# Kernel optimization log

Measured on AMD Instinct MI355X. Metric: run time of the kernel, lower is better.

Reference implementation:

```python
import jax, jax.numpy as jnp
import numpy as np

U, D, E, L = 100000, 10000, 500000, 100000
H, O, VC = 128, 64, 20
ED = H // 4  # emb_dim = hidden // 4


def setup_inputs() -> dict:
    key = jax.random.key(0)
    it = iter(jax.random.split(key, 60))
    def nrm(shape, s=0.1):
        return jax.random.normal(next(it), shape, jnp.float32) * s
    inp = {}
    inp["x_user"] = nrm((U, 3), 1.0)
    inp["x_dest"] = nrm((D, 1), 1.0)
    inp["edge_src"] = jax.random.randint(next(it), (E,), 0, U)
    inp["edge_dst"] = jax.random.randint(next(it), (E,), 0, D)
    inp["eattr_cat"] = jax.random.randint(next(it), (E, 3), 0, VC)
    inp["eattr_num"] = nrm((E, 3), 1.0)
    inp["label_src"] = jax.random.randint(next(it), (L,), 0, U)
    inp["label_dst"] = jax.random.randint(next(it), (L,), 0, D)
    inp["user_emb"] = nrm((U, H))
    inp["dest_emb"] = nrm((D, H))
    inp["Wuf"] = nrm((3, H)); inp["buf"] = jnp.zeros((H,), jnp.float32)
    inp["Wdf"] = nrm((1, H)); inp["bdf"] = jnp.zeros((H,), jnp.float32)
    inp["emb_acc"] = nrm((VC, ED)); inp["emb_trans"] = nrm((VC, ED)); inp["emb_season"] = nrm((VC, ED))
    inp["Wnum"] = nrm((3, ED)); inp["bnum"] = jnp.zeros((ED,), jnp.float32)
    inp["Weout"] = nrm((4 * ED, H)); inp["beout"] = jnp.zeros((H,), jnp.float32)
    inp["c1v_Ws"] = nrm((H, H)); inp["c1v_Wd"] = nrm((H, H)); inp["c1v_as"] = nrm((H,)); inp["c1v_ad"] = nrm((H,))
    inp["c1v_We"] = nrm((H, H)); inp["c1v_ae"] = nrm((H,)); inp["c1v_b"] = jnp.zeros((H,), jnp.float32)
    inp["c1r_Ws"] = nrm((H, H)); inp["c1r_Wd"] = nrm((H, H)); inp["c1r_as"] = nrm((H,)); inp["c1r_ad"] = nrm((H,)); inp["c1r_b"] = jnp.zeros((H,), jnp.float32)
    inp["c2v_W"] = nrm((H, H)); inp["c2v_as"] = nrm((H,)); inp["c2v_ad"] = nrm((H,)); inp["c2v_We"] = nrm((H, H)); inp["c2v_ae"] = nrm((H,)); inp["c2v_b"] = jnp.zeros((H,), jnp.float32)
    inp["c2r_W"] = nrm((H, H)); inp["c2r_as"] = nrm((H,)); inp["c2r_ad"] = nrm((H,)); inp["c2r_b"] = jnp.zeros((H,), jnp.float32)
    inp["Wmu"] = nrm((H, O)); inp["bmu"] = jnp.zeros((O,), jnp.float32)
    inp["Wls"] = nrm((H, O)); inp["bls"] = jnp.zeros((O,), jnp.float32)
    return inp


def gat(h_src, h_dst, src, dst, Ws, Wd, a_s, a_d, bias, n_dst, ef=None, We=None, ae=None):
    """PyG GATConv, heads=1, add_self_loops=False, bipartite (src->dst)."""
    xs = h_src @ Ws  # [Ns, H]
    xd = h_dst @ Wd  # [Nd, H]
    alpha = (xs * a_s).sum(-1)[src] + (xd * a_d).sum(-1)[dst]  # [E]
    if ef is not None:
        alpha = alpha + ((ef @ We) * ae).sum(-1)
    alpha = jnp.where(alpha > 0, alpha, 0.2 * alpha)  # leaky_relu(0.2)
    amax = jax.ops.segment_max(alpha, dst, num_segments=n_dst)
    ex = jnp.exp(alpha - amax[dst])
    denom = jax.ops.segment_sum(ex, dst, num_segments=n_dst)
    w = ex / (denom[dst] + 1e-16)  # segment softmax over incoming edges
    out = jax.ops.segment_sum(w[:, None] * xs[src], dst, num_segments=n_dst)
    return out + bias


def reference(x_user, x_dest, edge_src, edge_dst, eattr_cat, eattr_num, label_src, label_dst,
              user_emb, dest_emb, Wuf, buf, Wdf, bdf,
              emb_acc, emb_trans, emb_season, Wnum, bnum, Weout, beout,
              c1v_Ws, c1v_Wd, c1v_as, c1v_ad, c1v_We, c1v_ae, c1v_b,
              c1r_Ws, c1r_Wd, c1r_as, c1r_ad, c1r_b,
              c2v_W, c2v_as, c2v_ad, c2v_We, c2v_ae, c2v_b,
              c2r_W, c2r_as, c2r_ad, c2r_b,
              Wmu, bmu, Wls, bls):
    # node encoders (full-batch: arange ids == full embedding tables)
    h_user = user_emb + x_user @ Wuf + buf  # [U, H]
    h_dest = dest_emb + x_dest @ Wdf + bdf  # [D, H]
    # EdgeBehaviorEncoder
    ef = jnp.concatenate([emb_acc[eattr_cat[:, 0]], emb_trans[eattr_cat[:, 1]],
                          emb_season[eattr_cat[:, 2]], eattr_num @ Wnum + bnum], axis=1)
    ef = ef @ Weout + beout  # [E, H]
    # layer 1
    od1 = gat(h_user, h_dest, edge_src, edge_dst, c1v_Ws, c1v_Wd, c1v_as, c1v_ad, c1v_b, D, ef, c1v_We, c1v_ae)
    ou1 = gat(h_dest, h_user, edge_dst, edge_src, c1r_Ws, c1r_Wd, c1r_as, c1r_ad, c1r_b, U)
    hu = jax.nn.relu(ou1)
    hd = jax.nn.relu(od1)
    # layer 2 (int in_channels -> shared lin for src and dst)
    od2 = gat(hu, hd, edge_src, edge_dst, c2v_W, c2v_W, c2v_as, c2v_ad, c2v_b, D, ef, c2v_We, c2v_ae)
    ou2 = gat(hd, hu, edge_dst, edge_src, c2r_W, c2r_W, c2r_as, c2r_ad, c2r_b, U)
    zu = jax.nn.relu(ou2)
    zd = jax.nn.relu(od2)
    mu_u = zu @ Wmu + bmu
    mu_d = zd @ Wmu + bmu
    ls_u = zu @ Wls + bls
    ls_d = zd @ Wls + bls
    # eval mode: reparameterize returns mu; decode = dot product on label edges
    pred = (mu_u[label_src] * mu_d[label_dst]).sum(-1)  # [L]
    return pred, mu_u, mu_d, ls_u, ls_d
```

## Files before the change

kernel.cpp:

```cpp
#include <hip/hip_runtime.h>
#include <hip/hip_bf16.h>
#include <math.h>

#define H 128
#define CDIV(a,b) (((a)+(b)-1)/(b))

__device__ __forceinline__ float wave_reduce_sum(float v){
  #pragma unroll
  for (int off = 32; off > 0; off >>= 1) v += __shfl_down(v, off, 64);
  return v;
}
__device__ __forceinline__ float wave_reduce_max(float v){
  #pragma unroll
  for (int off = 32; off > 0; off >>= 1) v = fmaxf(v, __shfl_xor(v, off, 64));
  return v;
}

__global__ __launch_bounds__(128) void k_precompute(
    const float* c1v_Wd, const float* c1v_ad,
    const float* c1r_Wd, const float* c1r_ad,
    const float* c2v_W,  const float* c2v_ad,
    const float* c2r_W,  const float* c2r_ad,
    const float* c1v_We, const float* c1v_ae,
    const float* c2v_We, const float* c2v_ae,
    const float* Weout,  const float* beout,
    const float* emb_acc, const float* emb_trans, const float* emb_season,
    const float* Wnum, const float* bnum,
    const float* Wmu, const float* Wls, const float* bmu, const float* bls,
    float* sm)
{
  const int b = blockIdx.x, t = threadIdx.x;
  if (b < 4){
    const float* M; const float* a;
    if      (b == 0){ M = c1v_Wd; a = c1v_ad; }
    else if (b == 1){ M = c1r_Wd; a = c1r_ad; }
    else if (b == 2){ M = c2v_W;  a = c2v_ad; }
    else            { M = c2r_W;  a = c2r_ad; }
    float s = 0.f;
    for (int j = 0; j < H; ++j) s += M[t*H+j] * a[j];
    sm[b*H + t] = s;
  } else if (b == 4){
    __shared__ float ws[H], vs[H];
    for (int layer = 0; layer < 2; ++layer){
      const float* We = layer ? c2v_We : c1v_We;
      const float* ae = layer ? c2v_ae : c1v_ae;
      float w = 0.f;
      for (int j = 0; j < H; ++j) w += We[t*H+j] * ae[j];
      ws[t] = w;
      __syncthreads();
      float v = 0.f;
      for (int j = 0; j < H; ++j) v += Weout[t*H+j] * ws[j];
      vs[t] = v;
      __syncthreads();
      float* tab = sm + 512 + layer*64;
      if (t < 20){
        float s1 = 0.f, s2 = 0.f, s3 = 0.f;
        for (int i = 0; i < 32; ++i){
          s1 += emb_acc   [t*32+i] * vs[i];
          s2 += emb_trans [t*32+i] * vs[32+i];
          s3 += emb_season[t*32+i] * vs[64+i];
        }
        tab[t] = s1; tab[20+t] = s2; tab[40+t] = s3;
      }
      if (t < 3){
        float s = 0.f;
        for (int i = 0; i < 32; ++i) s += Wnum[t*32+i] * vs[96+i];
        tab[60+t] = s;
      }
      if (t == 0){
        float s = 0.f;
        for (int j = 0; j < H; ++j)  s += beout[j] * ws[j];
        for (int i = 0; i < 32; ++i) s += bnum[i] * vs[96+i];
        tab[63] = s;
      }
      __syncthreads();
    }
  } else {
    float* Wcat = sm + 768;
    for (int i = (b-5)*128 + t; i < 8192; i += 7*128){
      int h = i >> 6, o = i & 63;
      Wcat[h*H + o]      = Wmu[h*64 + o];
      Wcat[h*H + 64 + o] = Wls[h*64 + o];
    }
    if (b == 5) sm[640 + t] = (t < 64) ? bmu[t] : bls[t-64];
  }
}

__global__ __launch_bounds__(256) void k_enc_user(
    const float* __restrict__ emb, const float* __restrict__ x,
    const float* __restrict__ Wf, const float* __restrict__ b,
    const float* __restrict__ qd, float* __restrict__ out,
    float* __restrict__ sout, int N)
{
  int w = (blockIdx.x*blockDim.x + threadIdx.x) >> 6;
  int lane = threadIdx.x & 63;
  if (w >= N) return;
  const float2* emb2 = (const float2*)emb;
  const float2* Wf2  = (const float2*)Wf;
  float2 e  = emb2[(size_t)w*64 + lane];
  float x0 = x[w*3], x1 = x[w*3+1], x2 = x[w*3+2];
  float2 w0 = Wf2[lane], w1 = Wf2[64+lane], w2 = Wf2[128+lane];
  float2 bb = ((const float2*)b)[lane];
  float h0 = e.x + bb.x + x0*w0.x + x1*w1.x + x2*w2.x;
  float h1 = e.y + bb.y + x0*w0.y + x1*w1.y + x2*w2.y;
  ((float2*)out)[(size_t)w*64 + lane] = make_float2(h0, h1);
  float2 q = ((const float2*)qd)[lane];
  float p = wave_reduce_sum(h0*q.x + h1*q.y);
  if (lane == 0) sout[w] = p;
}

__global__ __launch_bounds__(256) void k_enc_dest(
    const float* __restrict__ emb, const float* __restrict__ x,
    const float* __restrict__ Wf, const float* __restrict__ b,
    const float* __restrict__ qd, float* __restrict__ out,
    float* __restrict__ sout, int N)
{
  int w = (blockIdx.x*blockDim.x + threadIdx.x) >> 6;
  int lane = threadIdx.x & 63;
  if (w >= N) return;
  float2 e  = ((const float2*)emb)[(size_t)w*64 + lane];
  float x0 = x[w];
  float2 w0 = ((const float2*)Wf)[lane];
  float2 bb = ((const float2*)b)[lane];
  float h0 = e.x + bb.x + x0*w0.x;
  float h1 = e.y + bb.y + x0*w0.y;
  ((float2*)out)[(size_t)w*64 + lane] = make_float2(h0, h1);
  float2 q = ((const float2*)qd)[lane];
  float p = wave_reduce_sum(h0*q.x + h1*q.y);
  if (lane == 0) sout[w] = p;
}

__global__ __launch_bounds__(256) void k_gemm128(
    const float* __restrict__ A, const float* __restrict__ W,
    const float* __restrict__ bias, const float* __restrict__ asv,
    float* __restrict__ sout,
    float* __restrict__ out0, float* __restrict__ out1,
    int ld0, int ld1, int N)
{
  __shared__ float Ws[64][128];
  __shared__ float Xs[64][132];
  __shared__ float red[64][17];
  const int tid = threadIdx.x;
  const int rb  = blockIdx.x * 64;
  const int tc  = tid & 15, tr = tid >> 4;
  const int c0  = tc * 8;
  float C[4][8] = {};
  for (int k0 = 0; k0 < 128; k0 += 64){
    for (int i = tid; i < 2048; i += 256){
      int k = i >> 5, c4 = i & 31;
      *(float4*)&Ws[k][c4*4] = *(const float4*)&W[(size_t)(k0+k)*128 + c4*4];
    }
    for (int i = tid; i < 1024; i += 256){
      int r = i >> 4, kg = i & 15;
      int row = rb + r;
      float4 v = make_float4(0.f,0.f,0.f,0.f);
      if (row < N) v = *(const float4*)&A[(size_t)row*128 + k0 + kg*4];
      *(float4*)&Xs[r][kg*4] = v;
    }
    __syncthreads();
    #pragma unroll 4
    for (int k = 0; k < 64; ++k){
      float4 w0 = *(float4*)&Ws[k][c0];
      float4 w1 = *(float4*)&Ws[k][c0+4];
      #pragma unroll
      for (int i = 0; i < 4; ++i){
        float x = Xs[tr*4+i][k];
        C[i][0] += x*w0.x; C[i][1] += x*w0.y; C[i][2] += x*w0.z; C[i][3] += x*w0.w;
        C[i][4] += x*w1.x; C[i][5] += x*w1.y; C[i][6] += x*w1.z; C[i][7] += x*w1.w;
      }
    }
    __syncthreads();
  }
  float4 b0 = make_float4(0,0,0,0), b1 = make_float4(0,0,0,0);
  if (bias){ b0 = *(const float4*)&bias[c0]; b1 = *(const float4*)&bias[c0+4]; }
  float4 a0 = make_float4(0,0,0,0), a1 = make_float4(0,0,0,0);
  if (asv){ a0 = *(const float4*)&asv[c0]; a1 = *(const float4*)&asv[c0+4]; }
  #pragma unroll
  for (int i = 0; i < 4; ++i){
    int row = rb + tr*4 + i;
    float s = 0.f;
    if (row < N){
      float4 v0 = make_float4(C[i][0]+b0.x, C[i][1]+b0.y, C[i][2]+b0.z, C[i][3]+b0.w);
      float4 v1 = make_float4(C[i][4]+b1.x, C[i][5]+b1.y, C[i][6]+b1.z, C[i][7]+b1.w);
      if (c0 < 64){
        *(float4*)&out0[(size_t)row*ld0 + c0]     = v0;
        *(float4*)&out0[(size_t)row*ld0 + c0 + 4] = v1;
      } else {
        *(float4*)&out1[(size_t)row*ld1 + (c0-64)]     = v0;
        *(float4*)&out1[(size_t)row*ld1 + (c0-64) + 4] = v1;
      }
      if (asv){
        s = C[i][0]*a0.x + C[i][1]*a0.y + C[i][2]*a0.z + C[i][3]*a0.w
          + C[i][4]*a1.x + C[i][5]*a1.y + C[i][6]*a1.z + C[i][7]*a1.w;
      }
    }
    if (asv) red[tr*4+i][tc] = s;
  }
  if (asv){
    __syncthreads();
    if (tid < 64){
      int row = rb + tid;
      if (row < N){
        float t = 0.f;
        #pragma unroll
        for (int j = 0; j < 16; ++j) t += red[tid][j];
        sout[row] = t;
      }
    }
  }
}

__global__ __launch_bounds__(256) void k_alpha_both(
    const int* __restrict__ esrc, const int* __restrict__ edst,
    const int* __restrict__ ecat, const float* __restrict__ enum_,
    const float* __restrict__ sUa, const float* __restrict__ sDa,
    const float* __restrict__ sDb, const float* __restrict__ sUb,
    const float* __restrict__ tab,
    const int* __restrict__ slotD, const int* __restrict__ slotU,
    float* __restrict__ alVs, float* __restrict__ alRs, int E)
{
  int e = blockIdx.x * blockDim.x + threadIdx.x;
  if (e >= E) return;
  int s = esrc[e], d = edst[e];
  float av = sUa[s] + sDa[d]
           + tab[ecat[e*3]] + tab[20 + ecat[e*3+1]] + tab[40 + ecat[e*3+2]]
           + enum_[e*3]*tab[60] + enum_[e*3+1]*tab[61] + enum_[e*3+2]*tab[62] + tab[63];
  av = av > 0.f ? av : 0.2f * av;
  alVs[slotD[e]] = av;
  float ar = sDb[d] + sUb[s];
  ar = ar > 0.f ? ar : 0.2f * ar;
  alRs[slotU[e]] = ar;
}

__global__ void k_zero2(int* a, int na, int* b, int nb){
  int i = blockIdx.x * blockDim.x + threadIdx.x;
  if (i < na) a[i] = 0;
  else if (i - na < nb) b[i - na] = 0;
}

__global__ void k_count_both(const int* __restrict__ esrc, const int* __restrict__ edst,
                             int* __restrict__ cntU, int* __restrict__ cntD, int E){
  int e = blockIdx.x * blockDim.x + threadIdx.x;
  if (e < E){ atomicAdd(&cntU[esrc[e]], 1); atomicAdd(&cntD[edst[e]], 1); }
}

__global__ __launch_bounds__(1024) void k_scan1(const int* __restrict__ cnt,
                                                int* __restrict__ offs,
                                                int* __restrict__ bsum, int n)
{
  __shared__ int wsum[16];
  const int tid = threadIdx.x, lane = tid & 63, wid = tid >> 6;
  const int i = blockIdx.x * 1024 + tid;
  int v = (i < n) ? cnt[i] : 0;
  int inc = v;
  #pragma unroll
  for (int d = 1; d < 64; d <<= 1){
    int t2 = __shfl_up(inc, d, 64);
    if (lane >= d) inc += t2;
  }
  if (lane == 63) wsum[wid] = inc;
  __syncthreads();
  if (tid < 16){
    int x = wsum[tid];
    #pragma unroll
    for (int d = 1; d < 16; d <<= 1){
      int t2 = __shfl_up(x, d, 16);
      if (tid >= d) x += t2;
    }
    wsum[tid] = x;
  }
  __syncthreads();
  int incl = ((wid > 0) ? wsum[wid-1] : 0) + inc;
  if (i < n) offs[i+1] = incl;
  if (tid == 0) bsum[blockIdx.x] = wsum[15];
}

__global__ __launch_bounds__(1024) void k_scan2(int* __restrict__ bsum, int nb)
{
  __shared__ int wsum[16];
  const int tid = threadIdx.x, lane = tid & 63, wid = tid >> 6;
  int v = (tid < nb) ? bsum[tid] : 0;
  int inc = v;
  #pragma unroll
  for (int d = 1; d < 64; d <<= 1){
    int t2 = __shfl_up(inc, d, 64);
    if (lane >= d) inc += t2;
  }
  if (lane == 63) wsum[wid] = inc;
  __syncthreads();
  if (tid < 16){
    int x = wsum[tid];
    #pragma unroll
    for (int d = 1; d < 16; d <<= 1){
      int t2 = __shfl_up(x, d, 16);
      if (tid >= d) x += t2;
    }
    wsum[tid] = x;
  }
  __syncthreads();
  int excl = ((wid > 0) ? wsum[wid-1] : 0) + inc - v;
  if (tid < nb) bsum[tid] = excl;
}

__global__ void k_scan3(const int* __restrict__ cnt, const int* __restrict__ bsum,
                        int* __restrict__ offs, int* __restrict__ cursor, int n)
{
  int i = blockIdx.x * blockDim.x + threadIdx.x;
  if (i >= n) return;
  int v = offs[i+1] + bsum[i >> 10];
  offs[i+1] = v;
  cursor[i] = v - cnt[i];
  if (i == 0) offs[0] = 0;
}

__global__ void k_scatter_both(const int* __restrict__ esrc, const int* __restrict__ edst,
                               int* __restrict__ curU, int* __restrict__ curD,
                               int* __restrict__ slotU, int* __restrict__ slotD,
                               int* __restrict__ srtOU, int* __restrict__ srtOD, int E)
{
  int e = blockIdx.x * blockDim.x + threadIdx.x;
  if (e >= E) return;
  int s = esrc[e], d = edst[e];
  int pD = atomicAdd(&curD[d], 1);
  slotD[e] = pD; srtOD[pD] = s;
  int pU = atomicAdd(&curU[s], 1);
  slotU[e] = pU; srtOU[pU] = d;
}

__global__ __launch_bounds__(256) void k_agg(
    const int* __restrict__ offs, const int* __restrict__ srt_other,
    const float* __restrict__ al, const float* __restrict__ xs,
    const float* __restrict__ bias, float* __restrict__ out,
    const float* __restrict__ qd, float* __restrict__ sout, int N)
{
  int w = (blockIdx.x*blockDim.x + threadIdx.x) >> 6;
  int lane = threadIdx.x & 63;
  if (w >= N) return;
  const int beg = offs[w], end = offs[w+1];

  float m = -1e30f;
  for (int i = beg + lane; i < end; i += 64) m = fmaxf(m, al[i]);
  m = wave_reduce_max(m);
  float s = 0.f;
  for (int i = beg + lane; i < end; i += 64) s += __expf(al[i] - m);
  s = wave_reduce_sum(s);
  s = __shfl(s, 0, 64);
  const float inv = 1.f / (s + 1e-16f);

  float a0 = 0.f, a1 = 0.f;
  const float2* xs2 = (const float2*)xs;
  for (int base = beg; base < end; base += 64){
    int nn = min(64, end - base);
    int o_l = 0; float w_l = 0.f;
    if (base + lane < end){
      o_l = srt_other[base + lane];
      w_l = __expf(al[base + lane] - m) * inv;
    }
    for (int j = 0; j < nn; ++j){
      int   oo = __shfl(o_l, j, 64);
      float ww = __shfl(w_l, j, 64);
      float2 v = xs2[(size_t)oo*64 + lane];
      a0 += ww * v.x; a1 += ww * v.y;
    }
  }
  float2 bb = ((const float2*)bias)[lane];
  float r0 = fmaxf(a0 + bb.x, 0.f);
  float r1 = fmaxf(a1 + bb.y, 0.f);
  ((float2*)out)[(size_t)w*64 + lane] = make_float2(r0, r1);
  if (qd){
    float2 q = ((const float2*)qd)[lane];
    float p = wave_reduce_sum(r0*q.x + r1*q.y);
    if (lane == 0) sout[w] = p;
  }
}

__global__ void k_pred(const int* __restrict__ ls, const int* __restrict__ ld,
                       const float* __restrict__ mu_u, const float* __restrict__ mu_d,
                       float* __restrict__ pred, int L)
{
  int wid  = (blockIdx.x * blockDim.x + threadIdx.x) >> 6;
  int lane = threadIdx.x & 63;
  if (wid >= L) return;
  float p = mu_u[(size_t)ls[wid]*64 + lane] * mu_d[(size_t)ld[wid]*64 + lane];
  p = wave_reduce_sum(p);
  if (lane == 0) pred[wid] = p;
}

extern "C" void kernel_launch(void* const* d_in, const int* in_sizes, int n_in,
                              void* d_out, int out_size, void* d_ws, size_t ws_size,
                              hipStream_t stream)
{
  (void)n_in; (void)out_size; (void)ws_size;
  const float* x_user    = (const float*)d_in[0];
  const float* x_dest    = (const float*)d_in[1];
  const int*   edge_src  = (const int*)d_in[2];
  const int*   edge_dst  = (const int*)d_in[3];
  const int*   eattr_cat = (const int*)d_in[4];
  const float* eattr_num = (const float*)d_in[5];
  const int*   label_src = (const int*)d_in[6];
  const int*   label_dst = (const int*)d_in[7];
  const float* user_emb  = (const float*)d_in[8];
  const float* dest_emb  = (const float*)d_in[9];
  const float* Wuf = (const float*)d_in[10]; const float* buf_ = (const float*)d_in[11];
  const float* Wdf = (const float*)d_in[12]; const float* bdf  = (const float*)d_in[13];
  const float* emb_acc    = (const float*)d_in[14];
  const float* emb_trans  = (const float*)d_in[15];
  const float* emb_season = (const float*)d_in[16];
  const float* Wnum = (const float*)d_in[17]; const float* bnum  = (const float*)d_in[18];
  const float* Weout = (const float*)d_in[19]; const float* beout = (const float*)d_in[20];
  const float* c1v_Ws = (const float*)d_in[21]; const float* c1v_Wd = (const float*)d_in[22];
  const float* c1v_as = (const float*)d_in[23]; const float* c1v_ad = (const float*)d_in[24];
  const float* c1v_We = (const float*)d_in[25]; const float* c1v_ae = (const float*)d_in[26];
  const float* c1v_b  = (const float*)d_in[27];
  const float* c1r_Ws = (const float*)d_in[28]; const float* c1r_Wd = (const float*)d_in[29];
  const float* c1r_as = (const float*)d_in[30]; const float* c1r_ad = (const float*)d_in[31];
  const float* c1r_b  = (const float*)d_in[32];
  const float* c2v_W  = (const float*)d_in[33]; const float* c2v_as = (const float*)d_in[34];
  const float* c2v_ad = (const float*)d_in[35]; const float* c2v_We = (const float*)d_in[36];
  const float* c2v_ae = (const float*)d_in[37]; const float* c2v_b  = (const float*)d_in[38];
  const float* c2r_W  = (const float*)d_in[39]; const float* c2r_as = (const float*)d_in[40];
  const float* c2r_ad = (const float*)d_in[41]; const float* c2r_b  = (const float*)d_in[42];
  const float* Wmu = (const float*)d_in[43]; const float* bmu = (const float*)d_in[44];
  const float* Wls = (const float*)d_in[45]; const float* bls = (const float*)d_in[46];

  const int U = in_sizes[0] / 3;
  const int D = in_sizes[1];
  const int E = in_sizes[2];
  const int L = in_sizes[6];
  const int O = 64;
  const int nbD = CDIV(D, 1024), nbU = CDIV(U, 1024);

  float* fw = (float*)d_ws;
  size_t off = 0;
  auto falloc = [&](size_t n)->float*{ float* p = fw + off; off += (n + 3) & ~(size_t)3; return p; };
  float* A    = falloc((size_t)U * H);
  float* BIG  = falloc((size_t)U * H);
  float* Bd   = falloc((size_t)D * H);
  float* SM   = falloc((size_t)D * H);
  float* alVs = falloc(E);
  float* alRs = falloc(E);
  float* sUa  = falloc(U);
  float* sUb  = falloc(U);
  float* sDa  = falloc(D);
  float* sDb  = falloc(D);
  float* sml  = falloc(17152);
  int* iw = (int*)(fw + off);
  size_t ioff = 0;
  auto ialloc = [&](size_t n)->int*{ int* p = iw + ioff; ioff += (n + 3) & ~(size_t)3; return p; };
  int* cntD  = ialloc(D);
  int* curD  = ialloc(D);
  int* offsD = ialloc((size_t)D + 1);
  int* cntU  = ialloc(U);
  int* curU  = ialloc(U);
  int* offsU = ialloc((size_t)U + 1);
  int* slotD = ialloc(E);
  int* slotU = ialloc(E);
  int* srtOD = ialloc(E);
  int* srtOU = ialloc(E);
  int* bsumD = ialloc(1024);
  int* bsumU = ialloc(1024);

  float* outp = (float*)d_out;
  float* pred = outp;
  float* mu_u = outp + L;
  float* mu_d = mu_u + (size_t)U * O;
  float* ls_u = mu_d + (size_t)D * O;
  float* ls_d = ls_u + (size_t)U * O;

  hipLaunchKernelGGL(k_precompute, dim3(12), dim3(128), 0, stream,
                     c1v_Wd, c1v_ad, c1r_Wd, c1r_ad, c2v_W, c2v_ad, c2r_W, c2r_ad,
                     c1v_We, c1v_ae, c2v_We, c2v_ae, Weout, beout,
                     emb_acc, emb_trans, emb_season, Wnum, bnum, Wmu, Wls, bmu, bls, sml);
  hipLaunchKernelGGL(k_enc_user, dim3(CDIV(U,4)), dim3(256), 0, stream,
                     user_emb, x_user, Wuf, buf_, sml+128, A, sUb, U);
  hipLaunchKernelGGL(k_enc_dest, dim3(CDIV(D,4)), dim3(256), 0, stream,
                     dest_emb, x_dest, Wdf, bdf, sml+0, Bd, sDa, D);

  hipLaunchKernelGGL(k_zero2, dim3(CDIV(U+D,256)), dim3(256), 0, stream, cntU, U, cntD, D);
  hipLaunchKernelGGL(k_count_both, dim3(CDIV(E,256)), dim3(256), 0, stream,
                     edge_src, edge_dst, cntU, cntD, E);
  hipLaunchKernelGGL(k_scan1, dim3(nbD), dim3(1024), 0, stream, cntD, offsD, bsumD, D);
  hipLaunchKernelGGL(k_scan1, dim3(nbU), dim3(1024), 0, stream, cntU, offsU, bsumU, U);
  hipLaunchKernelGGL(k_scan2, dim3(1), dim3(1024), 0, stream, bsumD, nbD);
  hipLaunchKernelGGL(k_scan2, dim3(1), dim3(1024), 0, stream, bsumU, nbU);
  hipLaunchKernelGGL(k_scan3, dim3(CDIV(D,256)), dim3(256), 0, stream, cntD, bsumD, offsD, curD, D);
  hipLaunchKernelGGL(k_scan3, dim3(CDIV(U,256)), dim3(256), 0, stream, cntU, bsumU, offsU, curU, U);
  hipLaunchKernelGGL(k_scatter_both, dim3(CDIV(E,256)), dim3(256), 0, stream,
                     edge_src, edge_dst, curU, curD, slotU, slotD, srtOU, srtOD, E);

  hipLaunchKernelGGL(k_gemm128, dim3(CDIV(U,64)), dim3(256), 0, stream,
                     A,  c1v_Ws, (const float*)nullptr, c1v_as, sUa, BIG, BIG+64, 128, 128, U);
  hipLaunchKernelGGL(k_gemm128, dim3(CDIV(D,64)), dim3(256), 0, stream,
                     Bd, c1r_Ws, (const float*)nullptr, c1r_as, sDb, SM, SM+64, 128, 128, D);
  hipLaunchKernelGGL(k_alpha_both, dim3(CDIV(E,256)), dim3(256), 0, stream,
                     edge_src, edge_dst, eattr_cat, eattr_num, sUa, sDa, sDb, sUb,
                     sml+512, slotD, slotU, alVs, alRs, E);
  hipLaunchKernelGGL(k_agg, dim3(CDIV(D,4)), dim3(256), 0, stream,
                     offsD, srtOD, alVs, BIG, c1v_b, Bd, sml+256, sDa, D);
  hipLaunchKernelGGL(k_agg, dim3(CDIV(U,4)), dim3(256), 0, stream,
                     offsU, srtOU, alRs, SM, c1r_b, A, sml+384, sUb, U);

  hipLaunchKernelGGL(k_gemm128, dim3(CDIV(U,64)), dim3(256), 0, stream,
                     A,  c2v_W, (const float*)nullptr, c2v_as, sUa, BIG, BIG+64, 128, 128, U);
  hipLaunchKernelGGL(k_gemm128, dim3(CDIV(D,64)), dim3(256), 0, stream,
                     Bd, c2r_W, (const float*)nullptr, c2r_as, sDb, SM, SM+64, 128, 128, D);
  hipLaunchKernelGGL(k_alpha_both, dim3(CDIV(E,256)), dim3(256), 0, stream,
                     edge_src, edge_dst, eattr_cat, eattr_num, sUa, sDa, sDb, sUb,
                     sml+576, slotD, slotU, alVs, alRs, E);
  hipLaunchKernelGGL(k_agg, dim3(CDIV(D,4)), dim3(256), 0, stream,
                     offsD, srtOD, alVs, BIG, c2v_b, Bd, (const float*)nullptr, (float*)nullptr, D);
  hipLaunchKernelGGL(k_agg, dim3(CDIV(U,4)), dim3(256), 0, stream,
                     offsU, srtOU, alRs, SM, c2r_b, A, (const float*)nullptr, (float*)nullptr, U);

  hipLaunchKernelGGL(k_gemm128, dim3(CDIV(U,64)), dim3(256), 0, stream,
                     A,  sml+768, sml+640, (const float*)nullptr, (float*)nullptr, mu_u, ls_u, 64, 64, U);
  hipLaunchKernelGGL(k_gemm128, dim3(CDIV(D,64)), dim3(256), 0, stream,
                     Bd, sml+768, sml+640, (const float*)nullptr, (float*)nullptr, mu_d, ls_d, 64, 64, D);
  hipLaunchKernelGGL(k_pred, dim3(CDIV((size_t)L*64,256)), dim3(256), 0, stream,
                     label_src, label_dst, mu_u, mu_d, pred, L);
}
```

Before: 916.8 us.

## Fuse attention logit computation into aggregation with precomputed edge records

Removes the separate per-edge alpha kernels that wrote logits into scattered CSR slots. The scatter kernel now stores, per destination-sorted edge, an int4 record holding the source index and the two layers' edge-attribute logit constants. The aggregation kernels recompute leaky-relu logits from the node scores using an online max/sum softmax with a wave merge. This drops the slot arrays, the logit buffers and two passes over all edges, but each logit is gathered and computed twice inside aggregation, and every D-side edge record is now 16 bytes.

```diff
diff --git a/kernel.cpp b/kernel.cpp
--- a/kernel.cpp
+++ b/kernel.cpp
@@ -10,10 +10,16 @@
   for (int off = 32; off > 0; off >>= 1) v += __shfl_down(v, off, 64);
   return v;
 }
-__device__ __forceinline__ float wave_reduce_max(float v){
+
+__device__ __forceinline__ void wave_merge_ms(float& m, float& s){
   #pragma unroll
-  for (int off = 32; off > 0; off >>= 1) v = fmaxf(v, __shfl_xor(v, off, 64));
-  return v;
+  for (int off = 32; off > 0; off >>= 1){
+    float m2 = __shfl_xor(m, off, 64);
+    float s2 = __shfl_xor(s, off, 64);
+    float mn = fmaxf(m, m2);
+    s = s*__expf(m - mn) + s2*__expf(m2 - mn);
+    m = mn;
+  }
 }
 
 __global__ __launch_bounds__(128) void k_precompute(
@@ -95,11 +101,11 @@
   int w = (blockIdx.x*blockDim.x + threadIdx.x) >> 6;
   int lane = threadIdx.x & 63;
   if (w >= N) return;
-  const float2* emb2 = (const float2*)emb;
-  const float2* Wf2  = (const float2*)Wf;
-  float2 e  = emb2[(size_t)w*64 + lane];
+  float2 e  = ((const float2*)emb)[(size_t)w*64 + lane];
   float x0 = x[w*3], x1 = x[w*3+1], x2 = x[w*3+2];
-  float2 w0 = Wf2[lane], w1 = Wf2[64+lane], w2 = Wf2[128+lane];
+  float2 w0 = ((const float2*)Wf)[lane];
+  float2 w1 = ((const float2*)Wf)[64+lane];
+  float2 w2 = ((const float2*)Wf)[128+lane];
   float2 bb = ((const float2*)b)[lane];
   float h0 = e.x + bb.x + x0*w0.x + x1*w1.x + x2*w2.x;
   float h1 = e.y + bb.y + x0*w0.y + x1*w1.y + x2*w2.y;
@@ -210,28 +216,6 @@
   }
 }
 
-__global__ __launch_bounds__(256) void k_alpha_both(
-    const int* __restrict__ esrc, const int* __restrict__ edst,
-    const int* __restrict__ ecat, const float* __restrict__ enum_,
-    const float* __restrict__ sUa, const float* __restrict__ sDa,
-    const float* __restrict__ sDb, const float* __restrict__ sUb,
-    const float* __restrict__ tab,
-    const int* __restrict__ slotD, const int* __restrict__ slotU,
-    float* __restrict__ alVs, float* __restrict__ alRs, int E)
-{
-  int e = blockIdx.x * blockDim.x + threadIdx.x;
-  if (e >= E) return;
-  int s = esrc[e], d = edst[e];
-  float av = sUa[s] + sDa[d]
-           + tab[ecat[e*3]] + tab[20 + ecat[e*3+1]] + tab[40 + ecat[e*3+2]]
-           + enum_[e*3]*tab[60] + enum_[e*3+1]*tab[61] + enum_[e*3+2]*tab[62] + tab[63];
-  av = av > 0.f ? av : 0.2f * av;
-  alVs[slotD[e]] = av;
-  float ar = sDb[d] + sUb[s];
-  ar = ar > 0.f ? ar : 0.2f * ar;
-  alRs[slotU[e]] = ar;
-}
-
 __global__ void k_zero2(int* a, int na, int* b, int nb){
   int i = blockIdx.x * blockDim.x + threadIdx.x;
   if (i < na) a[i] = 0;
@@ -313,52 +297,129 @@
   if (i == 0) offs[0] = 0;
 }
 
-__global__ void k_scatter_both(const int* __restrict__ esrc, const int* __restrict__ edst,
-                               int* __restrict__ curU, int* __restrict__ curD,
-                               int* __restrict__ slotU, int* __restrict__ slotD,
-                               int* __restrict__ srtOU, int* __restrict__ srtOD, int E)
+__global__ __launch_bounds__(256) void k_scatter_both(
+    const int* __restrict__ esrc, const int* __restrict__ edst,
+    const int* __restrict__ ecat, const float* __restrict__ enum_,
+    const float* __restrict__ tab1, const float* __restrict__ tab2,
+    int* __restrict__ curU, int* __restrict__ curD,
+    int4* __restrict__ recD, int* __restrict__ srtOU, int E)
 {
   int e = blockIdx.x * blockDim.x + threadIdx.x;
   if (e >= E) return;
   int s = esrc[e], d = edst[e];
+  int c0 = ecat[e*3], c1i = ecat[e*3+1], c2i = ecat[e*3+2];
+  float n0 = enum_[e*3], n1 = enum_[e*3+1], n2 = enum_[e*3+2];
+  float cA = tab1[c0] + tab1[20+c1i] + tab1[40+c2i]
+           + n0*tab1[60] + n1*tab1[61] + n2*tab1[62] + tab1[63];
+  float cB = tab2[c0] + tab2[20+c1i] + tab2[40+c2i]
+           + n0*tab2[60] + n1*tab2[61] + n2*tab2[62] + tab2[63];
   int pD = atomicAdd(&curD[d], 1);
-  slotD[e] = pD; srtOD[pD] = s;
+  recD[pD] = make_int4(s, __float_as_int(cA), __float_as_int(cB), 0);
   int pU = atomicAdd(&curU[s], 1);
-  slotU[e] = pU; srtOU[pU] = d;
-}
-
-__global__ __launch_bounds__(256) void k_agg(
-    const int* __restrict__ offs, const int* __restrict__ srt_other,
-    const float* __restrict__ al, const float* __restrict__ xs,
-    const float* __restrict__ bias, float* __restrict__ out,
-    const float* __restrict__ qd, float* __restrict__ sout, int N)
+  srtOU[pU] = d;
+}
+
+__global__ __launch_bounds__(256) void k_agg_v(
+    const int* __restrict__ offs, const int4* __restrict__ rec,
+    const float* __restrict__ gS, const float* __restrict__ selfS, int lsel,
+    const float* __restrict__ xs, const float* __restrict__ bias,
+    float* __restrict__ out, const float* __restrict__ qd,
+    float* __restrict__ sout, int N)
 {
   int w = (blockIdx.x*blockDim.x + threadIdx.x) >> 6;
   int lane = threadIdx.x & 63;
   if (w >= N) return;
   const int beg = offs[w], end = offs[w+1];
-
-  float m = -1e30f;
-  for (int i = beg + lane; i < end; i += 64) m = fmaxf(m, al[i]);
-  m = wave_reduce_max(m);
-  float s = 0.f;
-  for (int i = beg + lane; i < end; i += 64) s += __expf(al[i] - m);
-  s = wave_reduce_sum(s);
-  s = __shfl(s, 0, 64);
+  const float uni = selfS[w];
+
+  float m = -1e30f, s = 0.f;
+  for (int base = beg; base < end; base += 64){
+    int i = base + lane;
+    if (i < end){
+      int4 r = rec[i];
+      float a = gS[r.x] + uni + __int_as_float(lsel ? r.z : r.y);
+      a = a > 0.f ? a : 0.2f * a;
+      float mn = fmaxf(m, a);
+      s = s*__expf(m - mn) + __expf(a - mn);
+      m = mn;
+    }
+  }
+  wave_merge_ms(m, s);
   const float inv = 1.f / (s + 1e-16f);
 
   float a0 = 0.f, a1 = 0.f;
   const float2* xs2 = (const float2*)xs;
   for (int base = beg; base < end; base += 64){
+    int i = base + lane;
+    int o = 0; float wgt = 0.f;
+    if (i < end){
+      int4 r = rec[i];
+      o = r.x;
+      float a = gS[o] + uni + __int_as_float(lsel ? r.z : r.y);
+      a = a > 0.f ? a : 0.2f * a;
+      wgt = __expf(a - m) * inv;
+    }
     int nn = min(64, end - base);
-    int o_l = 0; float w_l = 0.f;
-    if (base + lane < end){
-      o_l = srt_other[base + lane];
-      w_l = __expf(al[base + lane] - m) * inv;
-    }
     for (int j = 0; j < nn; ++j){
-      int   oo = __shfl(o_l, j, 64);
-      float ww = __shfl(w_l, j, 64);
+      int   oo = __shfl(o, j, 64);
+      float ww = __shfl(wgt, j, 64);
+      float2 v = xs2[(size_t)oo*64 + lane];
+      a0 += ww * v.x; a1 += ww * v.y;
+    }
+  }
+  float2 bb = ((const float2*)bias)[lane];
+  float r0 = fmaxf(a0 + bb.x, 0.f);
+  float r1 = fmaxf(a1 + bb.y, 0.f);
+  ((float2*)out)[(size_t)w*64 + lane] = make_float2(r0, r1);
+  if (qd){
+    float2 q = ((const float2*)qd)[lane];
+    float p = wave_reduce_sum(r0*q.x + r1*q.y);
+    if (lane == 0) sout[w] = p;
+  }
+}
+
+__global__ __launch_bounds__(256) void k_agg_r(
+    const int* __restrict__ offs, const int* __restrict__ srtO,
+    const float* __restrict__ gS, const float* __restrict__ selfS,
+    const float* __restrict__ xs, const float* __restrict__ bias,
+    float* __restrict__ out, const float* __restrict__ qd,
+    float* __restrict__ sout, int N)
+{
+  int w = (blockIdx.x*blockDim.x + threadIdx.x) >> 6;
+  int lane = threadIdx.x & 63;
+  if (w >= N) return;
+  const int beg = offs[w], end = offs[w+1];
+  const float uni = selfS[w];
+
+  float m = -1e30f, s = 0.f;
+  for (int base = beg; base < end; base += 64){
+    int i = base + lane;
+    if (i < end){
+      float a = gS[srtO[i]] + uni;
+      a = a > 0.f ? a : 0.2f * a;
+      float mn = fmaxf(m, a);
+      s = s*__expf(m - mn) + __expf(a - mn);
+      m = mn;
+    }
+  }
+  wave_merge_ms(m, s);
+  const float inv = 1.f / (s + 1e-16f);
+
+  float a0 = 0.f, a1 = 0.f;
+  const float2* xs2 = (const float2*)xs;
+  for (int base = beg; base < end; base += 64){
+    int i = base + lane;
+    int o = 0; float wgt = 0.f;
+    if (i < end){
+      o = srtO[i];
+      float a = gS[o] + uni;
+      a = a > 0.f ? a : 0.2f * a;
+      wgt = __expf(a - m) * inv;
+    }
+    int nn = min(64, end - base);
+    for (int j = 0; j < nn; ++j){
+      int   oo = __shfl(o, j, 64);
+      float ww = __shfl(wgt, j, 64);
       float2 v = xs2[(size_t)oo*64 + lane];
       a0 += ww * v.x; a1 += ww * v.y;
     }
@@ -437,8 +498,6 @@
   float* BIG  = falloc((size_t)U * H);
   float* Bd   = falloc((size_t)D * H);
   float* SM   = falloc((size_t)D * H);
-  float* alVs = falloc(E);
-  float* alRs = falloc(E);
   float* sUa  = falloc(U);
   float* sUb  = falloc(U);
   float* sDa  = falloc(D);
@@ -447,16 +506,14 @@
   int* iw = (int*)(fw + off);
   size_t ioff = 0;
   auto ialloc = [&](size_t n)->int*{ int* p = iw + ioff; ioff += (n + 3) & ~(size_t)3; return p; };
+  int* recD  = ialloc((size_t)E * 4);
+  int* srtOU = ialloc(E);
   int* cntD  = ialloc(D);
   int* curD  = ialloc(D);
   int* offsD = ialloc((size_t)D + 1);
   int* cntU  = ialloc(U);
   int* curU  = ialloc(U);
   int* offsU = ialloc((size_t)U + 1);
-  int* slotD = ialloc(E);
-  int* slotU = ialloc(E);
-  int* srtOD = ialloc(E);
-  int* srtOU = ialloc(E);
   int* bsumD = ialloc(1024);
   int* bsumU = ialloc(1024);
 
@@ -486,31 +543,28 @@
   hipLaunchKernelGGL(k_scan3, dim3(CDIV(D,256)), dim3(256), 0, stream, cntD, bsumD, offsD, curD, D);
   hipLaunchKernelGGL(k_scan3, dim3(CDIV(U,256)), dim3(256), 0, stream, cntU, bsumU, offsU, curU, U);
   hipLaunchKernelGGL(k_scatter_both, dim3(CDIV(E,256)), dim3(256), 0, stream,
-                     edge_src, edge_dst, curU, curD, slotU, slotD, srtOU, srtOD, E);
+                     edge_src, edge_dst, eattr_cat, eattr_num, sml+512, sml+576,
+                     curU, curD, (int4*)recD, srtOU, E);
 
   hipLaunchKernelGGL(k_gemm128, dim3(CDIV(U,64)), dim3(256), 0, stream,
                      A,  c1v_Ws, (const float*)nullptr, c1v_as, sUa, BIG, BIG+64, 128, 128, U);
   hipLaunchKernelGGL(k_gemm128, dim3(CDIV(D,64)), dim3(256), 0, stream,
                      Bd, c1r_Ws, (const float*)nullptr, c1r_as, sDb, SM, SM+64, 128, 128, D);
-  hipLaunchKernelGGL(k_alpha_both, dim3(CDIV(E,256)), dim3(256), 0, stream,
-                     edge_src, edge_dst, eattr_cat, eattr_num, sUa, sDa, sDb, sUb,
-                     sml+512, slotD, slotU, alVs, alRs, E);
-  hipLaunchKernelGGL(k_agg, dim3(CDIV(D,4)), dim3(256), 0, stream,
-                     offsD, srtOD, alVs, BIG, c1v_b, Bd, sml+256, sDa, D);
-  hipLaunchKernelGGL(k_agg, dim3(CDIV(U,4)), dim3(256), 0, stream,
-                     offsU, srtOU, alRs, SM, c1r_b, A, sml+384, sUb, U);
+  hipLaunchKernelGGL(k_agg_v, dim3(CDIV(D,4)), dim3(256), 0, stream,
+                     offsD, (const int4*)recD, sUa, sDa, 0, BIG, c1v_b, Bd, sml+256, sDa, D);
+  hipLaunchKernelGGL(k_agg_r, dim3(CDIV(U,4)), dim3(256), 0, stream,
+                     offsU, srtOU, sDb, sUb, SM, c1r_b, A, sml+384, sUb, U);
 
   hipLaunchKernelGGL(k_gemm128, dim3(CDIV(U,64)), dim3(256), 0, stream,
                      A,  c2v_W, (const float*)nullptr, c2v_as, sUa, BIG, BIG+64, 128, 128, U);
   hipLaunchKernelGGL(k_gemm128, dim3(CDIV(D,64)), dim3(256), 0, stream,
                      Bd, c2r_W, (const float*)nullptr, c2r_as, sDb, SM, SM+64, 128, 128, D);
-  hipLaunchKernelGGL(k_alpha_both, dim3(CDIV(E,256)), dim3(256), 0, stream,
-                     edge_src, edge_dst, eattr_cat, eattr_num, sUa, sDa, sDb, sUb,
-                     sml+576, slotD, slotU, alVs, alRs, E);
-  hipLaunchKernelGGL(k_agg, dim3(CDIV(D,4)), dim3(256), 0, stream,
-                     offsD, srtOD, alVs, BIG, c2v_b, Bd, (const float*)nullptr, (float*)nullptr, D);
-  hipLaunchKernelGGL(k_agg, dim3(CDIV(U,4)), dim3(256), 0, stream,
-                     offsU, srtOU, alRs, SM, c2r_b, A, (const float*)nullptr, (float*)nullptr, U);
+  hipLaunchKernelGGL(k_agg_v, dim3(CDIV(D,4)), dim3(256), 0, stream,
+                     offsD, (const int4*)recD, sUa, sDa, 1, BIG, c2v_b, Bd,
+                     (const float*)nullptr, (float*)nullptr, D);
+  hipLaunchKernelGGL(k_agg_r, dim3(CDIV(U,4)), dim3(256), 0, stream,
+                     offsU, srtOU, sDb, sUb, SM, c2r_b, A,
+                     (const float*)nullptr, (float*)nullptr, U);
 
   hipLaunchKernelGGL(k_gemm128, dim3(CDIV(U,64)), dim3(256), 0, stream,
                      A,  sml+768, sml+640, (const float*)nullptr, (float*)nullptr, mu_u, ls_u, 64, 64, U);
```

Measured after the change: 875.5 us. 1.05x faster.
